# Performance work log

Measured on AMD Instinct MI355X. Metric: run time of the kernel, lower is better.

The kernel has to match this reference:

```python
import jax, jax.numpy as jnp
import numpy as np

# Gemma3 layer 0 (sliding-window layer -> local RoPE)
H = 8          # query heads
KVH = 4        # kv heads
DH = 256       # head dim
WINDOW = 1024  # sliding window
THETA_LOCAL = 10000.0
SCALE = 256.0 ** -0.5  # query_pre_attn_scalar**-0.5
EPS = 1e-6


def setup_inputs() -> dict:
    key = jax.random.key(0)
    ks = jax.random.split(key, 8)
    B, S, D = 1, 4096, 2560
    return {
        "hidden_states": jax.random.normal(ks[0], (B, S, D), jnp.float32),
        "attention_mask": jnp.ones((B, S), jnp.int32),
        "position_ids": jnp.broadcast_to(jnp.arange(S, dtype=jnp.int64), (B, S)),
        "wq": jax.random.normal(ks[1], (D, H * DH), jnp.float32) * 0.02,
        "wk": jax.random.normal(ks[2], (D, KVH * DH), jnp.float32) * 0.02,
        "wv": jax.random.normal(ks[3], (D, KVH * DH), jnp.float32) * 0.02,
        "wo": jax.random.normal(ks[4], (H * DH, D), jnp.float32) * 0.02,
        "q_norm_w": jnp.zeros((DH,), jnp.float32),  # Gemma RMSNorm uses (1 + w)
        "k_norm_w": jnp.zeros((DH,), jnp.float32),
    }


def _rms_norm(x, w):
    # Gemma-style RMSNorm over head_dim: x/rms * (1 + w)
    var = jnp.mean(jnp.square(x), axis=-1, keepdims=True)
    return x * jax.lax.rsqrt(var + EPS) * (1.0 + w)


def _rotate_half(x):
    x1, x2 = jnp.split(x, 2, axis=-1)
    return jnp.concatenate([-x2, x1], axis=-1)


def _rope(pos):
    # local RoPE (rope_type 'default', theta = rope_local_base_freq)
    inv_freq = 1.0 / (THETA_LOCAL ** (jnp.arange(0, DH, 2, dtype=jnp.float32) / DH))
    freqs = pos.astype(jnp.float32)[..., None] * inv_freq  # [B,S,DH/2]
    emb = jnp.concatenate([freqs, freqs], axis=-1)         # [B,S,DH]
    return jnp.cos(emb), jnp.sin(emb)


def reference(hidden_states, attention_mask, position_ids, wq, wk, wv, wo, q_norm_w, k_norm_w):
    B, S, D = hidden_states.shape
    # projections -> [B, heads, S, DH]
    q = (hidden_states @ wq).reshape(B, S, H, DH).transpose(0, 2, 1, 3)
    k = (hidden_states @ wk).reshape(B, S, KVH, DH).transpose(0, 2, 1, 3)
    v = (hidden_states @ wv).reshape(B, S, KVH, DH).transpose(0, 2, 1, 3)

    # per-head q/k RMSNorm (Gemma3)
    q = _rms_norm(q, q_norm_w)
    k = _rms_norm(k, k_norm_w)

    # RoPE
    cos, sin = _rope(position_ids)           # [B,S,DH]
    cos, sin = cos[:, None], sin[:, None]    # broadcast over heads
    q = q * cos + _rotate_half(q) * sin
    k = k * cos + _rotate_half(k) * sin

    # GQA: repeat kv heads
    rep = H // KVH
    k = jnp.repeat(k, rep, axis=1)
    v = jnp.repeat(v, rep, axis=1)

    # causal + sliding-window mask, combined with padding mask
    qi = jnp.arange(S)[:, None]
    ki = jnp.arange(S)[None, :]
    sw_mask = (ki <= qi) & (qi - ki < WINDOW)               # [S,S]
    pad = attention_mask.astype(bool)[:, None, None, :]     # [B,1,1,S]
    mask = sw_mask[None, None] & pad

    scores = jnp.einsum("bhqd,bhkd->bhqk", q, k) * SCALE
    scores = jnp.where(mask, scores, jnp.finfo(scores.dtype).min)
    probs = jax.nn.softmax(scores, axis=-1)

    out = jnp.einsum("bhqk,bhkd->bhqd", probs, v)            # [B,H,S,DH]
    out = out.transpose(0, 2, 1, 3).reshape(B, S, H * DH)
    return out @ wo
```

## Files before the change

### kernel.cpp

```cpp
#include <hip/hip_runtime.h>
#include <stdint.h>
#include <math.h>

typedef __bf16 bf16_t;
typedef __bf16 bf16x8 __attribute__((ext_vector_type(8)));
typedef __bf16 bf16x4 __attribute__((ext_vector_type(4)));
typedef float f32x4 __attribute__((ext_vector_type(4)));

#define GLD_LDS16(g, l)                                             \
    __builtin_amdgcn_global_load_lds(                               \
        (const __attribute__((address_space(1))) void*)(g),         \
        (__attribute__((address_space(3))) void*)(l), 16, 0, 0)

#define WAITV(N) asm volatile("s_waitcnt vmcnt(" #N ")" ::: "memory")
#define BARRIER() do { __builtin_amdgcn_sched_barrier(0);           \
                       __builtin_amdgcn_s_barrier();                \
                       __builtin_amdgcn_sched_barrier(0); } while (0)

__global__ __launch_bounds__(256)
void prep(const float* __restrict__ hs, bf16_t* __restrict__ hsb,
          const float* __restrict__ wq, const float* __restrict__ wk,
          const float* __restrict__ wv, bf16_t* __restrict__ Bh,
          float* __restrict__ ct, float* __restrict__ st)
{
    const int b = blockIdx.x;
    if (b >= 4608) {
        int i = (b - 4608) * 256 + threadIdx.x;
        float4 v = ((const float4*)hs)[i];
        bf16x4 o = { (bf16_t)v.x, (bf16_t)v.y, (bf16_t)v.z, (bf16_t)v.w };
        ((bf16x4*)hsb)[i] = o;
        return;
    }
    if (b >= 2560) {
        int t = (b - 2560) * 256 + threadIdx.x;
        int s = t >> 7, j = t & 127;
        double inv = exp2((double)j * (-13.28771237954945 / 128.0));
        double ang = fmod((double)s * inv, 6.283185307179586476925286766559);
        ct[t] = (float)cos(ang);
        st[t] = (float)sin(ang);
        return;
    }
    const float* src; bf16_t* dst; int C, bx, by;
    if (b < 1280)      { src = wq; dst = Bh;                          C = 2048; bx = b % 32;          by = b / 32; }
    else if (b < 1920) { src = wk; dst = Bh + (size_t)2048 * 2560;    C = 1024; bx = (b - 1280) % 16; by = (b - 1280) / 16; }
    else               { src = wv; dst = Bh + (size_t)3072 * 2560;    C = 1024; bx = (b - 1920) % 16; by = (b - 1920) / 16; }
    const int R = 2560;
    __shared__ float t[64][65];
    const int r0 = by * 64, c0 = bx * 64;
#pragma unroll
    for (int i = 0; i < 16; ++i) {
        int f = threadIdx.x + i * 256;
        int r = f >> 6, c = f & 63;
        t[r][c] = src[(size_t)(r0 + r) * C + c0 + c];
    }
    __syncthreads();
#pragma unroll
    for (int i = 0; i < 16; ++i) {
        int f = threadIdx.x + i * 256;
        int r = f >> 6, c = f & 63;
        dst[(size_t)(c0 + r) * R + r0 + c] = (bf16_t)t[c][r];
    }
}

__global__ __launch_bounds__(256)
void transpose_h(const float* __restrict__ in, bf16_t* __restrict__ out,
                 int R, int C)
{
    __shared__ float t[64][65];
    const int r0 = blockIdx.y * 64, c0 = blockIdx.x * 64;
#pragma unroll
    for (int i = 0; i < 16; ++i) {
        int f = threadIdx.x + i * 256;
        int r = f >> 6, c = f & 63;
        t[r][c] = in[(size_t)(r0 + r) * C + c0 + c];
    }
    __syncthreads();
#pragma unroll
    for (int i = 0; i < 16; ++i) {
        int f = threadIdx.x + i * 256;
        int r = f >> 6, c = f & 63;
        out[(size_t)(c0 + r) * R + r0 + c] = (bf16_t)t[c][r];
    }
}

__global__ __launch_bounds__(512, 2)
void gemm1(const bf16_t* __restrict__ A, const bf16_t* __restrict__ Bh,
           bf16_t* __restrict__ qb, bf16_t* __restrict__ kb,
           bf16_t* __restrict__ vt)
{
    __shared__ __attribute__((aligned(16))) char smem[131072];
    const int tid = threadIdx.x, lane = tid & 63, wid = tid >> 6;
    const int g = lane >> 4, c16 = lane & 15;
    const int wm = wid >> 2, wn = wid & 3;
    const int m0 = blockIdx.y * 256, n0 = blockIdx.x * 256;
    const int swz = c16 & 7;
    const int NT = 40;

    f32x4 acc[8][4];
#pragma unroll
    for (int m = 0; m < 8; ++m)
#pragma unroll
        for (int n = 0; n < 4; ++n) acc[m][n] = (f32x4)(0.f);

    auto STAGE_A = [&](int dbuf, int kt, int half) {
#pragma unroll
        for (int pl = 0; pl < 2; ++pl) {
            int c = pl * 512 + tid;
            int row = c >> 3, b = c & 7;
            GLD_LDS16(A + (size_t)(m0 + half * 128 + row) * 2560 + kt * 64
                        + ((b ^ (row & 7)) << 3),
                      smem + dbuf * 65536 + half * 16384
                        + (pl * 512 + wid * 64) * 16);
        }
    };
    auto STAGE_B = [&](int dbuf, int kt, int qp) {
#pragma unroll
        for (int pl = 0; pl < 2; ++pl) {
            int c = pl * 512 + tid;
            int u = c >> 3, b = c & 7;
            int row = ((u >> 5) << 6) + qp * 32 + (u & 31);
            int u0 = pl * 64 + wid * 8;
            int row0 = ((u0 >> 5) << 6) + qp * 32 + (u0 & 31);
            GLD_LDS16(Bh + (size_t)(n0 + row) * 2560 + kt * 64
                        + ((b ^ (row & 7)) << 3),
                      smem + dbuf * 65536 + 32768 + row0 * 128);
        }
    };

    STAGE_A(0, 0, 0); STAGE_A(0, 0, 1); STAGE_B(0, 0, 0); STAGE_B(0, 0, 1);
    WAITV(2);
    BARRIER();

    for (int t = 0; t < NT; ++t) {
        const int buf = t & 1, nbuf = buf ^ 1;
        const char* Ab = smem + buf * 65536;
        const char* Bb = smem + buf * 65536 + 32768;
        auto rdA = [&](int m, int kk) {
            return *(const bf16x8*)(Ab + (wm * 128 + m * 16 + c16) * 128
                                       + (((kk * 4 + g) ^ swz) << 4));
        };
        auto rdB = [&](int n, int kk) {
            return *(const bf16x8*)(Bb + (wn * 64 + n * 16 + c16) * 128
                                       + (((kk * 4 + g) ^ swz) << 4));
        };
        bf16x8 a[8], b0, b1, b2, b3;

#pragma unroll
        for (int m = 0; m < 8; ++m) a[m] = rdA(m, 0);
        b0 = rdB(0, 0); b1 = rdB(1, 0);
        if (t + 1 < NT) STAGE_A(nbuf, t + 1, 0);
        BARRIER();
        __builtin_amdgcn_s_setprio(1);
#pragma unroll
        for (int m = 0; m < 8; ++m) {
            acc[m][0] = __builtin_amdgcn_mfma_f32_16x16x32_bf16(a[m], b0, acc[m][0], 0, 0, 0);
            acc[m][1] = __builtin_amdgcn_mfma_f32_16x16x32_bf16(a[m], b1, acc[m][1], 0, 0, 0);
        }
        __builtin_amdgcn_s_setprio(0);
        if (t + 1 < NT) { WAITV(2); } else { WAITV(0); }
        BARRIER();

        b2 = rdB(2, 0); b3 = rdB(3, 0);
        if (t + 1 < NT) STAGE_A(nbuf, t + 1, 1);
        BARRIER();
        __builtin_amdgcn_s_setprio(1);
#pragma unroll
        for (int m = 0; m < 8; ++m) {
            acc[m][2] = __builtin_amdgcn_mfma_f32_16x16x32_bf16(a[m], b2, acc[m][2], 0, 0, 0);
            acc[m][3] = __builtin_amdgcn_mfma_f32_16x16x32_bf16(a[m], b3, acc[m][3], 0, 0, 0);
        }
        __builtin_amdgcn_s_setprio(0);
        BARRIER();

#pragma unroll
        for (int m = 0; m < 8; ++m) a[m] = rdA(m, 1);
        b0 = rdB(0, 1); b1 = rdB(1, 1);
        if (t + 1 < NT) STAGE_B(nbuf, t + 1, 0);
        BARRIER();
        __builtin_amdgcn_s_setprio(1);
#pragma unroll
        for (int m = 0; m < 8; ++m) {
            acc[m][0] = __builtin_amdgcn_mfma_f32_16x16x32_bf16(a[m], b0, acc[m][0], 0, 0, 0);
            acc[m][1] = __builtin_amdgcn_mfma_f32_16x16x32_bf16(a[m], b1, acc[m][1], 0, 0, 0);
        }
        __builtin_amdgcn_s_setprio(0);
        BARRIER();

        b2 = rdB(2, 1); b3 = rdB(3, 1);
        if (t + 1 < NT) STAGE_B(nbuf, t + 1, 1);
        BARRIER();
        __builtin_amdgcn_s_setprio(1);
#pragma unroll
        for (int m = 0; m < 8; ++m) {
            acc[m][2] = __builtin_amdgcn_mfma_f32_16x16x32_bf16(a[m], b2, acc[m][2], 0, 0, 0);
            acc[m][3] = __builtin_amdgcn_mfma_f32_16x16x32_bf16(a[m], b3, acc[m][3], 0, 0, 0);
        }
        __builtin_amdgcn_s_setprio(0);
        if (t + 1 < NT) WAITV(2);
        BARRIER();
    }

    if (n0 < 2048) {
#pragma unroll
        for (int m = 0; m < 8; ++m)
#pragma unroll
            for (int n = 0; n < 4; ++n) {
                int col = n0 + wn * 64 + n * 16 + c16;
                int rowb = m0 + wm * 128 + m * 16 + g * 4;
#pragma unroll
                for (int r = 0; r < 4; ++r)
                    qb[(size_t)(rowb + r) * 2048 + col] = (bf16_t)acc[m][n][r];
            }
    } else if (n0 < 3072) {
#pragma unroll
        for (int m = 0; m < 8; ++m)
#pragma unroll
            for (int n = 0; n < 4; ++n) {
                int col = n0 + wn * 64 + n * 16 + c16 - 2048;
                int rowb = m0 + wm * 128 + m * 16 + g * 4;
#pragma unroll
                for (int r = 0; r < 4; ++r)
                    kb[(size_t)(rowb + r) * 1024 + col] = (bf16_t)acc[m][n][r];
            }
    } else {
#pragma unroll
        for (int m = 0; m < 8; ++m)
#pragma unroll
            for (int n = 0; n < 4; ++n) {
                int d = n0 + wn * 64 + n * 16 + c16 - 3072;
                int rowb = m0 + wm * 128 + m * 16 + g * 4;
                int kvh_ = d >> 8, dd = d & 255;
                int kt = rowb >> 5, key = rowb & 31;
                bf16x4 hv;
#pragma unroll
                for (int r = 0; r < 4; ++r) hv[r] = (bf16_t)acc[m][n][r];
                size_t off = (size_t)kvh_ * 1048576 + (size_t)kt * 8192
                           + dd * 32 + (((key >> 3) ^ (dd & 3)) << 3) + (key & 7);
                *(bf16x4*)(vt + off) = hv;
            }
    }
}

__global__ __launch_bounds__(512, 2)
void gemm2p(const bf16_t* __restrict__ A, const bf16_t* __restrict__ Bh,
            float* __restrict__ C)
{
    __shared__ __attribute__((aligned(16))) char smem[131072];
    const int tid = threadIdx.x, lane = tid & 63, wid = tid >> 6;
    const int g = lane >> 4, c16 = lane & 15;
    const int wm = wid >> 2, wn = wid & 3;
    const int m0 = blockIdx.y * 256, n0 = blockIdx.x * 256;
    const int swz = c16 & 7;
    const int NT = 32;

    f32x4 acc[8][4];
#pragma unroll
    for (int m = 0; m < 8; ++m)
#pragma unroll
        for (int n = 0; n < 4; ++n) acc[m][n] = (f32x4)(0.f);

    auto STAGE_A = [&](int dbuf, int kt, int half) {
#pragma unroll
        for (int pl = 0; pl < 2; ++pl) {
            int c = pl * 512 + tid;
            int row = c >> 3, b = c & 7;
            GLD_LDS16(A + (size_t)(m0 + half * 128 + row) * 2048 + kt * 64
                        + ((b ^ (row & 7)) << 3),
                      smem + dbuf * 65536 + half * 16384
                        + (pl * 512 + wid * 64) * 16);
        }
    };
    auto STAGE_B = [&](int dbuf, int kt, int qp) {
#pragma unroll
        for (int pl = 0; pl < 2; ++pl) {
            int c = pl * 512 + tid;
            int u = c >> 3, b = c & 7;
            int row = ((u >> 5) << 6) + qp * 32 + (u & 31);
            int u0 = pl * 64 + wid * 8;
            int row0 = ((u0 >> 5) << 6) + qp * 32 + (u0 & 31);
            GLD_LDS16(Bh + (size_t)(n0 + row) * 2048 + kt * 64
                        + ((b ^ (row & 7)) << 3),
                      smem + dbuf * 65536 + 32768 + row0 * 128);
        }
    };

    STAGE_A(0, 0, 0); STAGE_A(0, 0, 1); STAGE_B(0, 0, 0); STAGE_B(0, 0, 1);
    WAITV(2);
    BARRIER();

    for (int t = 0; t < NT; ++t) {
        const int buf = t & 1, nbuf = buf ^ 1;
        const char* Ab = smem + buf * 65536;
        const char* Bb = smem + buf * 65536 + 32768;
        auto rdA = [&](int m, int kk) {
            return *(const bf16x8*)(Ab + (wm * 128 + m * 16 + c16) * 128
                                       + (((kk * 4 + g) ^ swz) << 4));
        };
        auto rdB = [&](int n, int kk) {
            return *(const bf16x8*)(Bb + (wn * 64 + n * 16 + c16) * 128
                                       + (((kk * 4 + g) ^ swz) << 4));
        };
        bf16x8 a[8], b0, b1, b2, b3;

#pragma unroll
        for (int m = 0; m < 8; ++m) a[m] = rdA(m, 0);
        b0 = rdB(0, 0); b1 = rdB(1, 0);
        if (t + 1 < NT) STAGE_A(nbuf, t + 1, 0);
        BARRIER();
        __builtin_amdgcn_s_setprio(1);
#pragma unroll
        for (int m = 0; m < 8; ++m) {
            acc[m][0] = __builtin_amdgcn_mfma_f32_16x16x32_bf16(a[m], b0, acc[m][0], 0, 0, 0);
            acc[m][1] = __builtin_amdgcn_mfma_f32_16x16x32_bf16(a[m], b1, acc[m][1], 0, 0, 0);
        }
        __builtin_amdgcn_s_setprio(0);
        if (t + 1 < NT) { WAITV(2); } else { WAITV(0); }
        BARRIER();

        b2 = rdB(2, 0); b3 = rdB(3, 0);
        if (t + 1 < NT) STAGE_A(nbuf, t + 1, 1);
        BARRIER();
        __builtin_amdgcn_s_setprio(1);
#pragma unroll
        for (int m = 0; m < 8; ++m) {
            acc[m][2] = __builtin_amdgcn_mfma_f32_16x16x32_bf16(a[m], b2, acc[m][2], 0, 0, 0);
            acc[m][3] = __builtin_amdgcn_mfma_f32_16x16x32_bf16(a[m], b3, acc[m][3], 0, 0, 0);
        }
        __builtin_amdgcn_s_setprio(0);
        BARRIER();

#pragma unroll
        for (int m = 0; m < 8; ++m) a[m] = rdA(m, 1);
        b0 = rdB(0, 1); b1 = rdB(1, 1);
        if (t + 1 < NT) STAGE_B(nbuf, t + 1, 0);
        BARRIER();
        __builtin_amdgcn_s_setprio(1);
#pragma unroll
        for (int m = 0; m < 8; ++m) {
            acc[m][0] = __builtin_amdgcn_mfma_f32_16x16x32_bf16(a[m], b0, acc[m][0], 0, 0, 0);
            acc[m][1] = __builtin_amdgcn_mfma_f32_16x16x32_bf16(a[m], b1, acc[m][1], 0, 0, 0);
        }
        __builtin_amdgcn_s_setprio(0);
        BARRIER();

        b2 = rdB(2, 1); b3 = rdB(3, 1);
        if (t + 1 < NT) STAGE_B(nbuf, t + 1, 1);
        BARRIER();
        __builtin_amdgcn_s_setprio(1);
#pragma unroll
        for (int m = 0; m < 8; ++m) {
            acc[m][2] = __builtin_amdgcn_mfma_f32_16x16x32_bf16(a[m], b2, acc[m][2], 0, 0, 0);
            acc[m][3] = __builtin_amdgcn_mfma_f32_16x16x32_bf16(a[m], b3, acc[m][3], 0, 0, 0);
        }
        __builtin_amdgcn_s_setprio(0);
        if (t + 1 < NT) WAITV(2);
        BARRIER();
    }

#pragma unroll
    for (int m = 0; m < 8; ++m)
#pragma unroll
        for (int n = 0; n < 4; ++n) {
            int col = n0 + wn * 64 + n * 16 + c16;
            int rowb = m0 + wm * 128 + m * 16 + g * 4;
#pragma unroll
            for (int r = 0; r < 4; ++r)
                C[(size_t)(rowb + r) * 2560 + col] = acc[m][n][r];
        }
}

__global__ __launch_bounds__(512)
void norm_qk(bf16_t* __restrict__ qb, const bf16_t* __restrict__ kraw,
             bf16_t* __restrict__ kb2, const float* __restrict__ qw,
             const float* __restrict__ kw, const float* __restrict__ ct,
             const float* __restrict__ st)
{
    const int s = blockIdx.x, t = threadIdx.x;
    if (t < 256) {
        const int h = t >> 5, l = t & 31;
        bf16_t* base = qb + (size_t)s * 2048 + h * 256 + l * 8;
        bf16x8 hv = *(const bf16x8*)base;
        float x[8], ss = 0.f;
#pragma unroll
        for (int j = 0; j < 8; ++j) { x[j] = (float)hv[j]; ss += x[j] * x[j]; }
#pragma unroll
        for (int mk = 1; mk < 32; mk <<= 1) ss += __shfl_xor(ss, mk);
        const float rs = rsqrtf(ss * (1.f / 256.f) + 1e-6f);
        float4 w0 = *(const float4*)(qw + l * 8);
        float4 w1 = *(const float4*)(qw + l * 8 + 4);
        float wa[8] = { w0.x, w0.y, w0.z, w0.w, w1.x, w1.y, w1.z, w1.w };
        float xn[8];
#pragma unroll
        for (int j = 0; j < 8; ++j) xn[j] = x[j] * rs * (1.f + wa[j]);
        const int d0 = (l * 8) & 127;
        float4 c0 = *(const float4*)(ct + s * 128 + d0);
        float4 c1 = *(const float4*)(ct + s * 128 + d0 + 4);
        float4 s0 = *(const float4*)(st + s * 128 + d0);
        float4 s1 = *(const float4*)(st + s * 128 + d0 + 4);
        float cc[8] = { c0.x, c0.y, c0.z, c0.w, c1.x, c1.y, c1.z, c1.w };
        float sn[8] = { s0.x, s0.y, s0.z, s0.w, s1.x, s1.y, s1.z, s1.w };
        const bool upper = (l >= 16);
        bf16x8 oh;
#pragma unroll
        for (int j = 0; j < 8; ++j) {
            float pn = __shfl_xor(xn[j], 16);
            float rot = upper ? pn : -pn;
            oh[j] = (bf16_t)(xn[j] * cc[j] + rot * sn[j]);
        }
        *(bf16x8*)base = oh;
    } else {
        const int tk = t - 256;
        const int h = tk >> 6, l = tk & 63;
        const bf16_t* base = kraw + (size_t)s * 1024 + h * 256 + l * 4;
        bf16x4 hv = *(const bf16x4*)base;
        float x[4], ss = 0.f;
#pragma unroll
        for (int j = 0; j < 4; ++j) { x[j] = (float)hv[j]; ss += x[j] * x[j]; }
#pragma unroll
        for (int mk = 1; mk < 64; mk <<= 1) ss += __shfl_xor(ss, mk);
        const float rs = rsqrtf(ss * (1.f / 256.f) + 1e-6f);
        float4 w0 = *(const float4*)(kw + l * 4);
        float wa[4] = { w0.x, w0.y, w0.z, w0.w };
        float xn[4];
#pragma unroll
        for (int j = 0; j < 4; ++j) xn[j] = x[j] * rs * (1.f + wa[j]);
        const int d0 = (l * 4) & 127;
        float4 c0 = *(const float4*)(ct + s * 128 + d0);
        float4 s0 = *(const float4*)(st + s * 128 + d0);
        float cc[4] = { c0.x, c0.y, c0.z, c0.w };
        float sn[4] = { s0.x, s0.y, s0.z, s0.w };
        const bool upper = (l >= 32);
        bf16x4 oh;
#pragma unroll
        for (int j = 0; j < 4; ++j) {
            float pn = __shfl_xor(xn[j], 32);
            float rot = upper ? pn : -pn;
            oh[j] = (bf16_t)(xn[j] * cc[j] + rot * sn[j]);
        }
        bf16_t* dst = kb2 + (size_t)h * 1048576 + (size_t)(s >> 5) * 8192
                    + (s & 31) * 256 + (((l >> 1) ^ (s & 7)) << 3) + (l & 1) * 4;
        *(bf16x4*)dst = oh;
    }
}

__global__ __launch_bounds__(256)
void attn_fwd8(const bf16_t* __restrict__ qb, const bf16_t* __restrict__ kb2,
               const bf16_t* __restrict__ vt2, bf16_t* __restrict__ attn)
{
    __shared__ __attribute__((aligned(16))) char smem[3 * 16384];
    __shared__ __attribute__((aligned(16))) bf16_t P[4][16][40];
    const int tid = threadIdx.x, lane = tid & 63, wid = tid >> 6;
    const int g = lane >> 4, c16 = lane & 15;
    const int h = blockIdx.x, kvh = h >> 1;
    const int by = blockIdx.y;
    const int qt = (by & 1) ? (63 - (by >> 1)) : (by >> 1);
    const int qrow0 = qt * 64 + wid * 16;

    const char* kslab = (const char*)kb2 + (size_t)kvh * 2097152;
    const char* vslab = (const char*)vt2 + (size_t)kvh * 2097152;

    bf16x8 qf[8];
#pragma unroll
    for (int c = 0; c < 8; ++c)
        qf[c] = *(const bf16x8*)(qb + (size_t)(qrow0 + c16) * 2048 + h * 256 + c * 32 + g * 8);

    float lrow[4] = { 0.f, 0.f, 0.f, 0.f };
    f32x4 acc[16];
#pragma unroll
    for (int nd = 0; nd < 16; ++nd) acc[nd] = (f32x4)(0.f);

    auto STAGE_K = [&](int buf, int kt) {
        char* Kd = smem + buf * 16384;
        const char* ks = kslab + (size_t)kt * 16384;
#pragma unroll
        for (int j = 0; j < 4; ++j)
            GLD_LDS16(ks + (size_t)(j * 256 + tid) * 16, Kd + (j * 256 + wid * 64) * 16);
    };
    auto STAGE_V = [&](int kt) {
        char* Vd = smem + 32768;
        const char* vs = vslab + (size_t)kt * 16384;
#pragma unroll
        for (int j = 0; j < 4; ++j)
            GLD_LDS16(vs + (size_t)(j * 256 + tid) * 16, Vd + (j * 256 + wid * 64) * 16);
    };

    const int ktb_lo = (qt >= 16) ? 2 * qt - 32 : 0;
    const int ktb_hi = 2 * qt + 1;
    int cur = 0;
    STAGE_K(0, ktb_lo);
    __syncthreads();

    const int swk = (c16 & 7) << 4;
    const int swv = (g ^ (c16 & 3)) << 4;
    const float S2 = 0.090168441f;

    for (int kt = ktb_lo; kt <= ktb_hi; ++kt) {
        STAGE_V(kt);
        if (kt < ktb_hi) STAGE_K(cur ^ 1, kt + 1);

        const bool rel = (kt * 32 <= qrow0 + 15) && (kt * 32 + 31 >= qrow0 - 1023);
        float p2[2][4];
        if (rel) {
            const char* Kc = smem + cur * 16384;
            f32x4 scA[2], scB[2];
#pragma unroll
            for (int n = 0; n < 2; ++n) { scA[n] = (f32x4)(0.f); scB[n] = (f32x4)(0.f); }
            __builtin_amdgcn_s_setprio(1);
#pragma unroll
            for (int n = 0; n < 2; ++n) {
                const char* kr = Kc + (n * 16 + c16) * 512;
#pragma unroll
                for (int c = 0; c < 4; ++c) {
                    bf16x8 kf = *(const bf16x8*)(kr + ((((c * 4 + g) << 4) ^ swk)));
                    scA[n] = __builtin_amdgcn_mfma_f32_16x16x32_bf16(qf[c], kf, scA[n], 0, 0, 0);
                }
#pragma unroll
                for (int c = 4; c < 8; ++c) {
                    bf16x8 kf = *(const bf16x8*)(kr + ((((c * 4 + g) << 4) ^ swk)));
                    scB[n] = __builtin_amdgcn_mfma_f32_16x16x32_bf16(qf[c], kf, scB[n], 0, 0, 0);
                }
            }
            __builtin_amdgcn_s_setprio(0);

            const bool fullv = (kt * 32 + 31 <= qrow0) && (kt * 32 >= qrow0 - 1008);
            if (fullv) {
#pragma unroll
                for (int n = 0; n < 2; ++n)
#pragma unroll
                    for (int r = 0; r < 4; ++r)
                        p2[n][r] = __builtin_amdgcn_exp2f((scA[n][r] + scB[n][r]) * S2);
            } else {
#pragma unroll
                for (int n = 0; n < 2; ++n) {
                    const int key = kt * 32 + n * 16 + c16;
#pragma unroll
                    for (int r = 0; r < 4; ++r) {
                        const int q = qrow0 + g * 4 + r;
                        bool valid = (key <= q) && (q - key < 1024);
                        float e = __builtin_amdgcn_exp2f((scA[n][r] + scB[n][r]) * S2);
                        p2[n][r] = valid ? e : 0.f;
                    }
                }
            }
#pragma unroll
            for (int n = 0; n < 2; ++n)
#pragma unroll
                for (int r = 0; r < 4; ++r) lrow[r] += p2[n][r];

#pragma unroll
            for (int n = 0; n < 2; ++n)
#pragma unroll
                for (int r = 0; r < 4; ++r)
                    P[wid][g * 4 + r][n * 16 + c16] = (bf16_t)p2[n][r];
        }
        __syncthreads();

        if (rel) {
            const char* Vc = smem + 32768;
            bf16x8 pa = *(const bf16x8*)(&P[wid][c16][g * 8]);
            __builtin_amdgcn_s_setprio(1);
#pragma unroll
            for (int nd = 0; nd < 16; ++nd) {
                bf16x8 vf = *(const bf16x8*)(Vc + (nd * 16 + c16) * 64 + swv);
                acc[nd] = __builtin_amdgcn_mfma_f32_16x16x32_bf16(pa, vf, acc[nd], 0, 0, 0);
            }
            __builtin_amdgcn_s_setprio(0);
        }
        __syncthreads();
        cur ^= 1;
    }

#pragma unroll
    for (int mk = 1; mk < 16; mk <<= 1)
#pragma unroll
        for (int r = 0; r < 4; ++r) lrow[r] += __shfl_xor(lrow[r], mk);

    float inv[4];
#pragma unroll
    for (int r = 0; r < 4; ++r) inv[r] = 1.f / lrow[r];
#pragma unroll
    for (int nd = 0; nd < 16; ++nd)
#pragma unroll
        for (int r = 0; r < 4; ++r) {
            int row = qrow0 + g * 4 + r;
            attn[(size_t)row * 2048 + h * 256 + nd * 16 + c16] =
                (bf16_t)(acc[nd][r] * inv[r]);
        }
}

extern "C" void kernel_launch(void* const* d_in, const int* in_sizes, int n_in,
                              void* d_out, int out_size, void* d_ws, size_t ws_size,
                              hipStream_t stream)
{
    (void)in_sizes; (void)n_in; (void)out_size; (void)ws_size;
    const float* hs  = (const float*)d_in[0];
    const float* wq  = (const float*)d_in[3];
    const float* wk  = (const float*)d_in[4];
    const float* wv  = (const float*)d_in[5];
    const float* wo  = (const float*)d_in[6];
    const float* qnw = (const float*)d_in[7];
    const float* knw = (const float*)d_in[8];

    char* ws = (char*)d_ws;
    bf16_t* hs_bf = (bf16_t*)(ws);
    bf16_t* qb    = (bf16_t*)(ws + 20971520);
    bf16_t* kraw  = (bf16_t*)(ws + 37748736);
    bf16_t* vt2   = (bf16_t*)(ws + 46137344);
    bf16_t* Bh    = (bf16_t*)(ws + 54525952);
    bf16_t* kb2   = (bf16_t*)(ws + 54525952);
    float*  ct    = (float*)(ws + 75497472);
    float*  st    = (float*)(ws + 77594624);
    bf16_t* attnb = (bf16_t*)(ws);
    bf16_t* woh   = (bf16_t*)(ws + 20971520);

    prep<<<14848, 256, 0, stream>>>(hs, hs_bf, wq, wk, wv, Bh, ct, st);

    gemm1<<<dim3(16, 16), 512, 0, stream>>>(hs_bf, Bh, qb, kraw, vt2);

    norm_qk<<<4096, 512, 0, stream>>>(qb, kraw, kb2, qnw, knw, ct, st);

    attn_fwd8<<<dim3(8, 64), 256, 0, stream>>>(qb, kb2, vt2, attnb);

    transpose_h<<<dim3(40, 32), 256, 0, stream>>>(wo, woh, 2048, 2560);
    gemm2p<<<dim3(10, 16), 512, 0, stream>>>(attnb, woh, (float*)d_out);
}
```

Measured before the change: 232.9 us.

## Fold wo transpose into norm_qk launch and remap GEMM block order across XCDs

Removes the separate transpose_h launch and runs the wo fp32-to-bf16 transpose as extra blocks of the norm_qk kernel, with the output moved to a workspace region that does not alias qb. Also permutes the block index in gemm1 and gemm2p so that consecutive hardware block IDs, which are dispatched round-robin across XCDs, map to neighbouring output tiles and share L2 reuse. The aim is to save one kernel launch and improve cache locality. The trade-off is that norm_qk blocks now reserve 33KB of shared memory even when they do not use it, which may lower their occupancy.

```diff
diff --git a/kernel.cpp b/kernel.cpp
--- a/kernel.cpp
+++ b/kernel.cpp
@@ -62,27 +62,6 @@
     }
 }
 
-__global__ __launch_bounds__(256)
-void transpose_h(const float* __restrict__ in, bf16_t* __restrict__ out,
-                 int R, int C)
-{
-    __shared__ float t[64][65];
-    const int r0 = blockIdx.y * 64, c0 = blockIdx.x * 64;
-#pragma unroll
-    for (int i = 0; i < 16; ++i) {
-        int f = threadIdx.x + i * 256;
-        int r = f >> 6, c = f & 63;
-        t[r][c] = in[(size_t)(r0 + r) * C + c0 + c];
-    }
-    __syncthreads();
-#pragma unroll
-    for (int i = 0; i < 16; ++i) {
-        int f = threadIdx.x + i * 256;
-        int r = f >> 6, c = f & 63;
-        out[(size_t)(c0 + r) * R + r0 + c] = (bf16_t)t[c][r];
-    }
-}
-
 __global__ __launch_bounds__(512, 2)
 void gemm1(const bf16_t* __restrict__ A, const bf16_t* __restrict__ Bh,
            bf16_t* __restrict__ qb, bf16_t* __restrict__ kb,
@@ -92,7 +71,9 @@
     const int tid = threadIdx.x, lane = tid & 63, wid = tid >> 6;
     const int g = lane >> 4, c16 = lane & 15;
     const int wm = wid >> 2, wn = wid & 3;
-    const int m0 = blockIdx.y * 256, n0 = blockIdx.x * 256;
+    const int bid = blockIdx.y * 16 + blockIdx.x;
+    const int nb = (bid & 7) * 32 + (bid >> 3);
+    const int m0 = (nb >> 4) * 256, n0 = (nb & 15) * 256;
     const int swz = c16 & 7;
     const int NT = 40;
 
@@ -249,7 +230,9 @@
     const int tid = threadIdx.x, lane = tid & 63, wid = tid >> 6;
     const int g = lane >> 4, c16 = lane & 15;
     const int wm = wid >> 2, wn = wid & 3;
-    const int m0 = blockIdx.y * 256, n0 = blockIdx.x * 256;
+    const int bid = blockIdx.y * 10 + blockIdx.x;
+    const int nb = (bid & 7) * 20 + (bid >> 3);
+    const int m0 = (nb / 10) * 256, n0 = (nb % 10) * 256;
     const int swz = c16 & 7;
     const int NT = 32;
 
@@ -373,9 +356,31 @@
 void norm_qk(bf16_t* __restrict__ qb, const bf16_t* __restrict__ kraw,
              bf16_t* __restrict__ kb2, const float* __restrict__ qw,
              const float* __restrict__ kw, const float* __restrict__ ct,
-             const float* __restrict__ st)
+             const float* __restrict__ st, const float* __restrict__ wo,
+             bf16_t* __restrict__ woh)
 {
+    __shared__ float tt[2][64][65];
     const int s = blockIdx.x, t = threadIdx.x;
+    if (s >= 4096) {
+        const int half = t >> 8, tl = t & 255;
+        const int tileIdx = (s - 4096) * 2 + half;
+        const int bx = tileIdx % 40, by = tileIdx / 40;
+        const int r0 = by * 64, c0 = bx * 64;
+#pragma unroll
+        for (int i = 0; i < 16; ++i) {
+            int f = tl + i * 256;
+            int r = f >> 6, c = f & 63;
+            tt[half][r][c] = wo[(size_t)(r0 + r) * 2560 + c0 + c];
+        }
+        __syncthreads();
+#pragma unroll
+        for (int i = 0; i < 16; ++i) {
+            int f = tl + i * 256;
+            int r = f >> 6, c = f & 63;
+            woh[(size_t)(c0 + r) * 2048 + r0 + c] = (bf16_t)tt[half][c][r];
+        }
+        return;
+    }
     if (t < 256) {
         const int h = t >> 5, l = t & 31;
         bf16_t* base = qb + (size_t)s * 2048 + h * 256 + l * 8;
@@ -608,19 +613,18 @@
     bf16_t* vt2   = (bf16_t*)(ws + 46137344);
     bf16_t* Bh    = (bf16_t*)(ws + 54525952);
     bf16_t* kb2   = (bf16_t*)(ws + 54525952);
+    bf16_t* woh   = (bf16_t*)(ws + 62914560);
     float*  ct    = (float*)(ws + 75497472);
     float*  st    = (float*)(ws + 77594624);
     bf16_t* attnb = (bf16_t*)(ws);
-    bf16_t* woh   = (bf16_t*)(ws + 20971520);
 
     prep<<<14848, 256, 0, stream>>>(hs, hs_bf, wq, wk, wv, Bh, ct, st);
 
     gemm1<<<dim3(16, 16), 512, 0, stream>>>(hs_bf, Bh, qb, kraw, vt2);
 
-    norm_qk<<<4096, 512, 0, stream>>>(qb, kraw, kb2, qnw, knw, ct, st);
+    norm_qk<<<4736, 512, 0, stream>>>(qb, kraw, kb2, qnw, knw, ct, st, wo, woh);
 
     attn_fwd8<<<dim3(8, 64), 256, 0, stream>>>(qb, kb2, vt2, attnb);
 
-    transpose_h<<<dim3(40, 32), 256, 0, stream>>>(wo, woh, 2048, 2560);
     gemm2p<<<dim3(10, 16), 512, 0, stream>>>(attnb, woh, (float*)d_out);
 }
```

Result: no change. 230.6 us, median of 2 (-1.0%).
